# Kernel tuning notes

Measured on AMD Instinct MI355X. Metric: run time of the kernel, lower is better.

Reference implementation:

```python
import jax, jax.numpy as jnp
import numpy as np

B, S, HIDDEN = 4, 2048, 1024
HEADS = 16
D = HIDDEN // HEADS  # att_size = 64
SCALE = D ** -0.5


def setup_inputs() -> dict:
    key = jax.random.key(0)
    k_x, k_qkv, k_out = jax.random.split(key, 3)
    x = jax.random.normal(k_x, (B, S, HIDDEN), dtype=jnp.float32)
    # torch Linear weights: (out_features, in_features); xavier-uniform init
    lim_qkv = np.sqrt(6.0 / (HIDDEN + 3 * HIDDEN))
    W_qkv = jax.random.uniform(k_qkv, (3 * HEADS * D, HIDDEN), dtype=jnp.float32,
                               minval=-lim_qkv, maxval=lim_qkv)
    lim_out = np.sqrt(6.0 / (HIDDEN + HIDDEN))
    W_out = jax.random.uniform(k_out, (HIDDEN, HEADS * D), dtype=jnp.float32,
                               minval=-lim_out, maxval=lim_out)
    return {"x": x, "W_qkv": W_qkv, "W_out": W_out}


def reference(x, W_qkv, W_out):
    b, s, _ = x.shape
    # fused QKV projection; feature layout along output dim is [3][heads][d]
    qkv = jnp.einsum('bsh,fh->bsf', x, W_qkv).reshape(b, s, 3, HEADS, D)
    q = qkv[:, :, 0].transpose(0, 2, 1, 3) * SCALE  # [b, H, s, d]
    k = qkv[:, :, 1].transpose(0, 2, 1, 3)
    v = qkv[:, :, 2].transpose(0, 2, 1, 3)
    scores = jnp.einsum('bhqd,bhkd->bhqk', q, k)
    attn = jax.nn.softmax(scores, axis=-1)
    ctx = jnp.einsum('bhqk,bhkd->bhqd', attn, v)
    ctx = ctx.transpose(0, 2, 1, 3).reshape(b, s, HEADS * D)
    return jnp.einsum('bsf,hf->bsh', ctx, W_out)
```

## Files before the change

kernel.cpp:

```cpp
#include <hip/hip_runtime.h>
#include <hip/hip_bf16.h>
#include <stdint.h>
#include <math.h>


using half8  = __attribute__((ext_vector_type(8))) _Float16;
using half4  = __attribute__((ext_vector_type(4))) _Float16;
using f32x4  = __attribute__((ext_vector_type(4))) float;
using f32x16 = __attribute__((ext_vector_type(16))) float;
using u32x4  = __attribute__((ext_vector_type(4))) unsigned int;

#define HID   1024
#define NHEAD 16
#define HDIM  64
#define NB    4
#define SEQ   2048
#define MROWS (NB*SEQ)
#define NKTH  16

typedef __attribute__((address_space(1))) const void* gas_t;
typedef __attribute__((address_space(3))) void*       las_t;

__global__ void conv_h(const float* __restrict__ in, _Float16* __restrict__ out,
                       int n4, int nscale, float qs){
  int i = blockIdx.x * 256 + threadIdx.x;
  if (i >= n4) return;
  f32x4 v = *(const f32x4*)(in + (size_t)i*4);
  int row = (i*4) >> 10;
  if (row < nscale){ v[0]*=qs; v[1]*=qs; v[2]*=qs; v[3]*=qs; }
  half4 o = { (_Float16)v[0], (_Float16)v[1], (_Float16)v[2], (_Float16)v[3] };
  *(half4*)(out + (size_t)i*4) = o;
}

__device__ __forceinline__ void stage_tile(const _Float16* __restrict__ g,
                                           char* lds, int t, int wid){
#pragma unroll
  for (int i = 0; i < 4; ++i){
    int tl  = i*256 + t;
    int row = tl >> 3;
    int srcb = (((tl & 7) << 4)) ^ ((row & 7) << 4);
    __builtin_amdgcn_global_load_lds(
        (gas_t)((const char*)(g + (size_t)row*1024) + srcb),
        (las_t)(lds + (i*256 + wid*64)*16), 16, 0, 0);
  }
}

template<int EPI>
__global__ __launch_bounds__(256)
void gemmh(const _Float16* __restrict__ A, const _Float16* __restrict__ B,
           float* __restrict__ C,
           _Float16* __restrict__ qo, _Float16* __restrict__ ko,
           _Float16* __restrict__ vo, int N)
{
  __shared__ __align__(16) char lA[128*128];
  __shared__ __align__(16) char lB[128*128];
  int t = threadIdx.x, lane = t & 63, wid = t >> 6;
  int fq = lane >> 4, fr = lane & 15;
  int m0 = blockIdx.x * 128, n0 = blockIdx.y * 128;
  int wm = (wid >> 1) * 64, wn = (wid & 1) * 64;
  f32x4 acc[4][4] = {};

  for (int kt = 0; kt < NKTH; ++kt){
    stage_tile(A + (size_t)m0*1024 + kt*64, lA, t, wid);
    stage_tile(B + (size_t)n0*1024 + kt*64, lB, t, wid);
    __syncthreads();
#pragma unroll
    for (int kc = 0; kc < 2; ++kc){
      half8 af[4], bf[4];
#pragma unroll
      for (int mi = 0; mi < 4; ++mi){
        int row = wm + mi*16 + fr;
        af[mi] = *(const half8*)(lA + row*128 + ((kc*64 + fq*16) ^ ((row&7)<<4)));
      }
#pragma unroll
      for (int ni = 0; ni < 4; ++ni){
        int row = wn + ni*16 + fr;
        bf[ni] = *(const half8*)(lB + row*128 + ((kc*64 + fq*16) ^ ((row&7)<<4)));
      }
      __builtin_amdgcn_s_setprio(1);
#pragma unroll
      for (int mi = 0; mi < 4; ++mi)
#pragma unroll
        for (int ni = 0; ni < 4; ++ni)
          acc[mi][ni] = __builtin_amdgcn_mfma_f32_16x16x32_f16(af[mi], bf[ni],
                                                               acc[mi][ni], 0, 0, 0);
      __builtin_amdgcn_s_setprio(0);
    }
    __syncthreads();
  }

  if (EPI == 0){
#pragma unroll
    for (int mi = 0; mi < 4; ++mi)
#pragma unroll
      for (int ni = 0; ni < 4; ++ni)
#pragma unroll
        for (int r = 0; r < 4; ++r){
          int m = m0 + wm + mi*16 + fq*4 + r;
          int n = n0 + wn + ni*16 + fr;
          C[(size_t)m*N + n] = acc[mi][ni][r];
        }
  } else {
    int cls = n0 >> 10;
#pragma unroll
    for (int mi = 0; mi < 4; ++mi)
#pragma unroll
      for (int ni = 0; ni < 4; ++ni)
#pragma unroll
        for (int r = 0; r < 4; ++r){
          int m = m0 + wm + mi*16 + fq*4 + r;
          int n = n0 + wn + ni*16 + fr;
          float v = acc[mi][ni][r];
          int b = m >> 11, s = m & 2047;
          int nn = n & 1023;
          int h = nn >> 6, d2 = nn & 63;
          int bh = b*NHEAD + h;
          if (cls == 0){
            qo[((size_t)bh*SEQ + s)*HDIM + d2] = (_Float16)v;
          } else if (cls == 1){
            int kb = s >> 5, l31 = s & 31;
            int c = d2 >> 4, hi8 = (d2 >> 3) & 1, e = d2 & 7;
            ko[((((size_t)bh*64 + kb)*4 + c)*64 + hi8*32 + l31)*8 + e] = (_Float16)v;
          } else {
            int kb = s >> 5, kk = s & 31;
            int kh = kk >> 4, hv = (kk >> 3) & 1, e = kk & 7;
            int dh = d2 >> 5, lv = d2 & 31;
            vo[((((size_t)bh*64 + kb)*4 + dh*2 + kh)*64 + hv*32 + lv)*8 + e] = (_Float16)v;
          }
        }
  }
}

#define MFMA32H(A,B,C) __builtin_amdgcn_mfma_f32_32x32x16_f16(A, B, C, 0, 0, 0)

__global__ __launch_bounds__(256)
void attn_fused(const _Float16* __restrict__ Qs, const _Float16* __restrict__ KF,
                const _Float16* __restrict__ VF, _Float16* __restrict__ ctx)
{
  int t = threadIdx.x, lane = t & 63, wid = t >> 6;
  int l31 = lane & 31, hi8 = lane >> 5;

  int orig = blockIdx.x;
  int wg = (orig & 7) * 128 + (orig >> 3);
  int bh = wg >> 4, qt = wg & 15;

  const _Float16* Qb = Qs + (size_t)bh*SEQ*HDIM;
  const _Float16* Kb = KF + ((size_t)bh*64*4*64)*8 + (size_t)lane*8;
  const _Float16* Vb = VF + ((size_t)bh*64*4*64)*8 + (size_t)lane*8;
  int qg = qt*128 + wid*32 + l31;

  half8 qf[4];
#pragma unroll
  for (int c = 0; c < 4; ++c)
    qf[c] = *(const half8*)&Qb[(size_t)qg*HDIM + c*16 + hi8*8];

  f32x16 av0 = {}, av1 = {};
  f32x4 lq = {};

  for (int k32 = 0; k32 < SEQ/32; ++k32){
    const _Float16* kp = Kb + (size_t)k32*2048;
    const _Float16* vp = Vb + (size_t)k32*2048;

    half8 vf00 = *(const half8*)(vp);
    half8 vf01 = *(const half8*)(vp + 512);
    half8 vf10 = *(const half8*)(vp + 1024);
    half8 vf11 = *(const half8*)(vp + 1536);
    half8 kf0 = *(const half8*)(kp);
    half8 kf1 = *(const half8*)(kp + 512);
    half8 kf2 = *(const half8*)(kp + 1024);
    half8 kf3 = *(const half8*)(kp + 1536);

    f32x16 sc;
#pragma unroll
    for (int i = 0; i < 16; ++i) sc[i] = -4.0f;
    __builtin_amdgcn_s_setprio(1);
    sc = MFMA32H(kf0, qf[0], sc);
    sc = MFMA32H(kf1, qf[1], sc);
    sc = MFMA32H(kf2, qf[2], sc);
    sc = MFMA32H(kf3, qf[3], sc);
    __builtin_amdgcn_s_setprio(0);

#pragma unroll
    for (int i = 0; i < 16; ++i) sc[i] = __builtin_amdgcn_exp2f(sc[i]);
    lq[0] += (sc[0]+sc[1])   + (sc[2]+sc[3]);
    lq[1] += (sc[4]+sc[5])   + (sc[6]+sc[7]);
    lq[2] += (sc[8]+sc[9])   + (sc[10]+sc[11]);
    lq[3] += (sc[12]+sc[13]) + (sc[14]+sc[15]);

    uint32_t a0,a1,a2,a3,b0,b1,b2,b3;
    asm("v_cvt_pkrtz_f16_f32 %0, %1, %2" : "=v"(a0) : "v"(sc[0]),  "v"(sc[1]));
    asm("v_cvt_pkrtz_f16_f32 %0, %1, %2" : "=v"(a1) : "v"(sc[2]),  "v"(sc[3]));
    asm("v_cvt_pkrtz_f16_f32 %0, %1, %2" : "=v"(a2) : "v"(sc[4]),  "v"(sc[5]));
    asm("v_cvt_pkrtz_f16_f32 %0, %1, %2" : "=v"(a3) : "v"(sc[6]),  "v"(sc[7]));
    asm("v_cvt_pkrtz_f16_f32 %0, %1, %2" : "=v"(b0) : "v"(sc[8]),  "v"(sc[9]));
    asm("v_cvt_pkrtz_f16_f32 %0, %1, %2" : "=v"(b1) : "v"(sc[10]), "v"(sc[11]));
    asm("v_cvt_pkrtz_f16_f32 %0, %1, %2" : "=v"(b2) : "v"(sc[12]), "v"(sc[13]));
    asm("v_cvt_pkrtz_f16_f32 %0, %1, %2" : "=v"(b3) : "v"(sc[14]), "v"(sc[15]));
    asm volatile("v_permlane32_swap_b32 %0, %1" : "+v"(a0), "+v"(a2));
    asm volatile("v_permlane32_swap_b32 %0, %1" : "+v"(a1), "+v"(a3));
    asm volatile("v_permlane32_swap_b32 %0, %1" : "+v"(b0), "+v"(b2));
    asm volatile("v_permlane32_swap_b32 %0, %1" : "+v"(b1), "+v"(b3));
    u32x4 w0; w0.x=a0; w0.y=a1; w0.z=a2; w0.w=a3;
    u32x4 w1; w1.x=b0; w1.y=b1; w1.z=b2; w1.w=b3;
    half8 pf0 = __builtin_bit_cast(half8, w0);
    half8 pf1 = __builtin_bit_cast(half8, w1);

    __builtin_amdgcn_s_setprio(1);
    av0 = MFMA32H(vf00, pf0, av0);
    av0 = MFMA32H(vf01, pf1, av0);
    av1 = MFMA32H(vf10, pf0, av1);
    av1 = MFMA32H(vf11, pf1, av1);
    __builtin_amdgcn_s_setprio(0);
  }

  float lh = (lq[0]+lq[1]) + (lq[2]+lq[3]);
  float lt = lh + __shfl_xor(lh, 32);
  float linv = 1.0f / lt;
  int b = bh >> 4, h = bh & 15;
  _Float16* orow = ctx + ((size_t)b*SEQ + qg)*HID + h*64;
#pragma unroll
  for (int g = 0; g < 4; ++g){
    half4 o0, o1;
#pragma unroll
    for (int i = 0; i < 4; ++i){
      o0[i] = (_Float16)(av0[g*4+i]*linv);
      o1[i] = (_Float16)(av1[g*4+i]*linv);
    }
    *(half4*)(orow + g*8 + hi8*4)      = o0;
    *(half4*)(orow + 32 + g*8 + hi8*4) = o1;
  }
}

extern "C" void kernel_launch(void* const* d_in, const int* in_sizes, int n_in,
                              void* d_out, int out_size, void* d_ws, size_t ws_size,
                              hipStream_t stream)
{
  const float* x  = (const float*)d_in[0];
  const float* Wq = (const float*)d_in[1];
  const float* Wo = (const float*)d_in[2];
  float* out = (float*)d_out;
  char* ws = (char*)d_ws;

  _Float16* XH  = (_Float16*)(ws);
  _Float16* WQH = (_Float16*)(ws + 16777216);
  _Float16* QH  = (_Float16*)(ws + 23068672);
  _Float16* KFb = (_Float16*)(ws + 39845888);
  _Float16* VFb = (_Float16*)(ws + 56623104);
  _Float16* CH  = (_Float16*)(ws + 73400320);
  _Float16* WOH = (_Float16*)(ws + 90177536);

  const float qs = 0.125f * 1.4426950408889634f;

  conv_h<<<(MROWS*HID/4)/256, 256, 0, stream>>>(x,  XH,  MROWS*HID/4, 0, 1.0f);
  conv_h<<<(3*HID*HID/4)/256, 256, 0, stream>>>(Wq, WQH, 3*HID*HID/4, HID, qs);
  conv_h<<<(HID*HID/4)/256, 256, 0, stream>>>(Wo, WOH, HID*HID/4, 0, 1.0f);

  gemmh<1><<<dim3(64, 24), 256, 0, stream>>>(XH, WQH, nullptr, QH, KFb, VFb, 3*HID);

  attn_fused<<<dim3(1024), 256, 0, stream>>>(QH, KFb, VFb, CH);

  gemmh<0><<<dim3(64, 8), 256, 0, stream>>>(CH, WOH, out, nullptr, nullptr, nullptr, HID);
}
```

Before: 211.5 us.

## Stage K/V tiles through double-buffered LDS with async global-to-LDS loads

```diff
diff --git a/kernel.cpp b/kernel.cpp
--- a/kernel.cpp
+++ b/kernel.cpp
@@ -133,10 +133,30 @@
 
 #define MFMA32H(A,B,C) __builtin_amdgcn_mfma_f32_32x32x16_f16(A, B, C, 0, 0, 0)
 
+__device__ __forceinline__ void stage_kv(const char* Kg, const char* Vg, int kt,
+                                         char* dK, char* dV, int t, int wid){
+  const char* ks = Kg + (size_t)kt*8192;
+  const char* vs = Vg + (size_t)kt*8192;
+#pragma unroll
+  for (int i = 0; i < 2; ++i){
+    int sl = i*256 + t;
+    __builtin_amdgcn_global_load_lds((gas_t)(ks + sl*16),
+                                     (las_t)(dK + (i*256 + wid*64)*16), 16, 0, 0);
+  }
+#pragma unroll
+  for (int i = 0; i < 2; ++i){
+    int sl = i*256 + t;
+    __builtin_amdgcn_global_load_lds((gas_t)(vs + sl*16),
+                                     (las_t)(dV + (i*256 + wid*64)*16), 16, 0, 0);
+  }
+}
+
 __global__ __launch_bounds__(256)
 void attn_fused(const _Float16* __restrict__ Qs, const _Float16* __restrict__ KF,
                 const _Float16* __restrict__ VF, _Float16* __restrict__ ctx)
 {
+  __shared__ __align__(16) char lK[2][8192];
+  __shared__ __align__(16) char lV[2][8192];
   int t = threadIdx.x, lane = t & 63, wid = t >> 6;
   int l31 = lane & 31, hi8 = lane >> 5;
 
@@ -145,8 +165,8 @@
   int bh = wg >> 4, qt = wg & 15;
 
   const _Float16* Qb = Qs + (size_t)bh*SEQ*HDIM;
-  const _Float16* Kb = KF + ((size_t)bh*64*4*64)*8 + (size_t)lane*8;
-  const _Float16* Vb = VF + ((size_t)bh*64*4*64)*8 + (size_t)lane*8;
+  const char* Kg = (const char*)(KF + (size_t)bh*64*4*64*8);
+  const char* Vg = (const char*)(VF + (size_t)bh*64*4*64*8);
   int qg = qt*128 + wid*32 + l31;
 
   half8 qf[4];
@@ -154,63 +174,74 @@
   for (int c = 0; c < 4; ++c)
     qf[c] = *(const half8*)&Qb[(size_t)qg*HDIM + c*16 + hi8*8];
 
+  f32x16 BIAS;
+#pragma unroll
+  for (int i = 0; i < 16; ++i) BIAS[i] = -4.0f;
+
   f32x16 av0 = {}, av1 = {};
   f32x4 lq = {};
 
-  for (int k32 = 0; k32 < SEQ/32; ++k32){
-    const _Float16* kp = Kb + (size_t)k32*2048;
-    const _Float16* vp = Vb + (size_t)k32*2048;
-
-    half8 vf00 = *(const half8*)(vp);
-    half8 vf01 = *(const half8*)(vp + 512);
-    half8 vf10 = *(const half8*)(vp + 1024);
-    half8 vf11 = *(const half8*)(vp + 1536);
-    half8 kf0 = *(const half8*)(kp);
-    half8 kf1 = *(const half8*)(kp + 512);
-    half8 kf2 = *(const half8*)(kp + 1024);
-    half8 kf3 = *(const half8*)(kp + 1536);
-
-    f32x16 sc;
-#pragma unroll
-    for (int i = 0; i < 16; ++i) sc[i] = -4.0f;
-    __builtin_amdgcn_s_setprio(1);
-    sc = MFMA32H(kf0, qf[0], sc);
-    sc = MFMA32H(kf1, qf[1], sc);
-    sc = MFMA32H(kf2, qf[2], sc);
-    sc = MFMA32H(kf3, qf[3], sc);
-    __builtin_amdgcn_s_setprio(0);
-
-#pragma unroll
-    for (int i = 0; i < 16; ++i) sc[i] = __builtin_amdgcn_exp2f(sc[i]);
-    lq[0] += (sc[0]+sc[1])   + (sc[2]+sc[3]);
-    lq[1] += (sc[4]+sc[5])   + (sc[6]+sc[7]);
-    lq[2] += (sc[8]+sc[9])   + (sc[10]+sc[11]);
-    lq[3] += (sc[12]+sc[13]) + (sc[14]+sc[15]);
-
-    uint32_t a0,a1,a2,a3,b0,b1,b2,b3;
-    asm("v_cvt_pkrtz_f16_f32 %0, %1, %2" : "=v"(a0) : "v"(sc[0]),  "v"(sc[1]));
-    asm("v_cvt_pkrtz_f16_f32 %0, %1, %2" : "=v"(a1) : "v"(sc[2]),  "v"(sc[3]));
-    asm("v_cvt_pkrtz_f16_f32 %0, %1, %2" : "=v"(a2) : "v"(sc[4]),  "v"(sc[5]));
-    asm("v_cvt_pkrtz_f16_f32 %0, %1, %2" : "=v"(a3) : "v"(sc[6]),  "v"(sc[7]));
-    asm("v_cvt_pkrtz_f16_f32 %0, %1, %2" : "=v"(b0) : "v"(sc[8]),  "v"(sc[9]));
-    asm("v_cvt_pkrtz_f16_f32 %0, %1, %2" : "=v"(b1) : "v"(sc[10]), "v"(sc[11]));
-    asm("v_cvt_pkrtz_f16_f32 %0, %1, %2" : "=v"(b2) : "v"(sc[12]), "v"(sc[13]));
-    asm("v_cvt_pkrtz_f16_f32 %0, %1, %2" : "=v"(b3) : "v"(sc[14]), "v"(sc[15]));
-    asm volatile("v_permlane32_swap_b32 %0, %1" : "+v"(a0), "+v"(a2));
-    asm volatile("v_permlane32_swap_b32 %0, %1" : "+v"(a1), "+v"(a3));
-    asm volatile("v_permlane32_swap_b32 %0, %1" : "+v"(b0), "+v"(b2));
-    asm volatile("v_permlane32_swap_b32 %0, %1" : "+v"(b1), "+v"(b3));
-    u32x4 w0; w0.x=a0; w0.y=a1; w0.z=a2; w0.w=a3;
-    u32x4 w1; w1.x=b0; w1.y=b1; w1.z=b2; w1.w=b3;
-    half8 pf0 = __builtin_bit_cast(half8, w0);
-    half8 pf1 = __builtin_bit_cast(half8, w1);
-
-    __builtin_amdgcn_s_setprio(1);
-    av0 = MFMA32H(vf00, pf0, av0);
-    av0 = MFMA32H(vf01, pf1, av0);
-    av1 = MFMA32H(vf10, pf0, av1);
-    av1 = MFMA32H(vf11, pf1, av1);
-    __builtin_amdgcn_s_setprio(0);
+  stage_kv(Kg, Vg, 0, lK[0], lV[0], t, wid);
+  int cur = 0;
+
+  for (int kt = 0; kt < 32; ++kt){
+    asm volatile("s_waitcnt vmcnt(0)" ::: "memory");
+    __builtin_amdgcn_s_barrier();
+    if (kt + 1 < 32) stage_kv(Kg, Vg, kt + 1, lK[cur ^ 1], lV[cur ^ 1], t, wid);
+
+#pragma unroll
+    for (int st = 0; st < 2; ++st){
+      const char* kp = lK[cur] + st*4096 + lane*16;
+      const char* vp = lV[cur] + st*4096 + lane*16;
+      half8 kf0 = *(const half8*)(kp);
+      half8 kf1 = *(const half8*)(kp + 1024);
+      half8 kf2 = *(const half8*)(kp + 2048);
+      half8 kf3 = *(const half8*)(kp + 3072);
+      half8 vf00 = *(const half8*)(vp);
+      half8 vf01 = *(const half8*)(vp + 1024);
+      half8 vf10 = *(const half8*)(vp + 2048);
+      half8 vf11 = *(const half8*)(vp + 3072);
+
+      __builtin_amdgcn_s_setprio(1);
+      f32x16 sc = MFMA32H(kf0, qf[0], BIAS);
+      sc = MFMA32H(kf1, qf[1], sc);
+      sc = MFMA32H(kf2, qf[2], sc);
+      sc = MFMA32H(kf3, qf[3], sc);
+      __builtin_amdgcn_s_setprio(0);
+
+#pragma unroll
+      for (int i = 0; i < 16; ++i) sc[i] = __builtin_amdgcn_exp2f(sc[i]);
+      lq[0] += (sc[0]+sc[1])   + (sc[2]+sc[3]);
+      lq[1] += (sc[4]+sc[5])   + (sc[6]+sc[7]);
+      lq[2] += (sc[8]+sc[9])   + (sc[10]+sc[11]);
+      lq[3] += (sc[12]+sc[13]) + (sc[14]+sc[15]);
+
+      uint32_t a0,a1,a2,a3,b0,b1,b2,b3;
+      asm("v_cvt_pkrtz_f16_f32 %0, %1, %2" : "=v"(a0) : "v"(sc[0]),  "v"(sc[1]));
+      asm("v_cvt_pkrtz_f16_f32 %0, %1, %2" : "=v"(a1) : "v"(sc[2]),  "v"(sc[3]));
+      asm("v_cvt_pkrtz_f16_f32 %0, %1, %2" : "=v"(a2) : "v"(sc[4]),  "v"(sc[5]));
+      asm("v_cvt_pkrtz_f16_f32 %0, %1, %2" : "=v"(a3) : "v"(sc[6]),  "v"(sc[7]));
+      asm("v_cvt_pkrtz_f16_f32 %0, %1, %2" : "=v"(b0) : "v"(sc[8]),  "v"(sc[9]));
+      asm("v_cvt_pkrtz_f16_f32 %0, %1, %2" : "=v"(b1) : "v"(sc[10]), "v"(sc[11]));
+      asm("v_cvt_pkrtz_f16_f32 %0, %1, %2" : "=v"(b2) : "v"(sc[12]), "v"(sc[13]));
+      asm("v_cvt_pkrtz_f16_f32 %0, %1, %2" : "=v"(b3) : "v"(sc[14]), "v"(sc[15]));
+      asm volatile("v_permlane32_swap_b32 %0, %1" : "+v"(a0), "+v"(a2));
+      asm volatile("v_permlane32_swap_b32 %0, %1" : "+v"(a1), "+v"(a3));
+      asm volatile("v_permlane32_swap_b32 %0, %1" : "+v"(b0), "+v"(b2));
+      asm volatile("v_permlane32_swap_b32 %0, %1" : "+v"(b1), "+v"(b3));
+      u32x4 w0; w0.x=a0; w0.y=a1; w0.z=a2; w0.w=a3;
+      u32x4 w1; w1.x=b0; w1.y=b1; w1.z=b2; w1.w=b3;
+      half8 pf0 = __builtin_bit_cast(half8, w0);
+      half8 pf1 = __builtin_bit_cast(half8, w1);
+
+      __builtin_amdgcn_s_setprio(1);
+      av0 = MFMA32H(vf00, pf0, av0);
+      av0 = MFMA32H(vf01, pf1, av0);
+      av1 = MFMA32H(vf10, pf0, av1);
+      av1 = MFMA32H(vf11, pf1, av1);
+      __builtin_amdgcn_s_setprio(0);
+    }
+    cur ^= 1;
   }
 
   float lh = (lq[0]+lq[1]) + (lq[2]+lq[3]);
```

Result: faster. 206.5 us (-2.4%).
